# Performance work log

Measured on AMD Instinct MI355X. Metric: run time of the kernel, lower is better.

Reference implementation:

```python
import jax, jax.numpy as jnp
from jax import lax
import numpy as np

SCALE, IN_C, OUT_C, KER, R = 2, 64, 64, 3, 4

def _tconv(x, w, b, s, ker):
    # PyTorch ConvTranspose2d(w: [in,out,k,k], padding=ker//2, stride=s, output_padding=s-1)
    # as a fractionally-strided conv: flip kernel, swap in/out channel axes.
    wk = jnp.flip(jnp.transpose(w, (1, 0, 2, 3)), (2, 3))  # [out,in,k,k]
    p = ker // 2
    y = lax.conv_general_dilated(
        x, wk, window_strides=(1, 1),
        padding=[(p, p + s - 1), (p, p + s - 1)],
        lhs_dilation=(s, s),
        dimension_numbers=('NCHW', 'OIHW', 'NCHW'))
    return y + b[None, :, None, None]

def setup_inputs() -> dict:
    key = jax.random.key(0)
    ks = jax.random.split(key, 8)
    B, H, W = 4, 256, 256
    x = jax.random.normal(ks[0], (B, IN_C, H, W), jnp.float32)
    m = (jax.random.uniform(ks[1], (B, 1, H * SCALE, W * SCALE)) > 0.5).astype(jnp.float32)
    inv_mask = 1.0 - m
    # params (std per module init; exact std irrelevant for correctness)
    high_w = jax.random.normal(ks[2], (IN_C, OUT_C, KER, KER), jnp.float32) * 0.001
    high_b = jnp.zeros((OUT_C,), jnp.float32)
    low1_w = jax.random.normal(ks[3], (IN_C // R, IN_C, 1, 1), jnp.float32) * np.sqrt(2.0 / (IN_C // R))
    low1_b = jnp.zeros((IN_C // R,), jnp.float32)
    low2_w = jax.random.normal(ks[4], (IN_C // R, OUT_C, KER, KER), jnp.float32) * 0.001
    low2_b = jnp.zeros((OUT_C,), jnp.float32)
    return {"x": x, "mask": m, "inv_mask": inv_mask,
            "high_w": high_w, "high_b": high_b,
            "low1_w": low1_w, "low1_b": low1_b,
            "low2_w": low2_w, "low2_b": low2_b}

def reference(x, mask, inv_mask, high_w, high_b, low1_w, low1_b, low2_w, low2_b):
    # high branch: full transposed conv, masked per upsampled pixel
    high = _tconv(x, high_w, high_b, SCALE, KER) * mask  # [B,out,2H,2W]
    # low branch: 1x1 channel reduction then transposed conv, complementary mask
    low = jnp.einsum('bchw,oc->bohw', x, low1_w[:, :, 0, 0]) + low1_b[None, :, None, None]
    low = _tconv(low, low2_w, low2_b, SCALE, KER) * inv_mask
    return high + low
```

## Files before the change

### kernel.cpp

```cpp
#include <hip/hip_runtime.h>


typedef unsigned short u16;
typedef unsigned int   u32;
typedef __bf16 bf16x8 __attribute__((ext_vector_type(8)));
typedef u16    u16x8  __attribute__((ext_vector_type(8)));
typedef float  f32x4  __attribute__((ext_vector_type(4)));

#define DEV static __device__ __forceinline__

DEV u16   f2bf(float f){ u32 u = __builtin_bit_cast(u32, f); u += 0x7FFF + ((u >> 16) & 1); return (u16)(u >> 16); }
DEV bf16x8 asb(u16x8 v){ return __builtin_bit_cast(bf16x8, v); }
#define MF(acc, A, B) acc = __builtin_amdgcn_mfma_f32_16x16x32_bf16(asb(A), asb(B), acc, 0, 0, 0)

__global__ __launch_bounds__(256) void wprep(const float* __restrict__ hw, const float* __restrict__ lw,
                                             const float* __restrict__ l1w,
                                             u16* __restrict__ whi, u16* __restrict__ wlo,
                                             u16* __restrict__ w1f)
{
  int t = blockIdx.x * 256 + threadIdx.x;
  if (t < 36864) {
    int e = t & 7, lane = (t >> 3) & 63, tile = (t >> 9) & 3, Q = (t >> 11) & 1, tap = t >> 12;
    int q = lane >> 4, n = lane & 15;
    int c = 32 * Q + 8 * q + e, och = 16 * tile + n;
    whi[t] = f2bf(hw[(c * 64 + och) * 9 + tap]);
  } else if (t < 47104) {
    int t2 = t - 36864;
    int e = t2 & 7, lane = (t2 >> 3) & 63, tile = (t2 >> 9) & 3, f = t2 >> 11;
    int q = lane >> 4, n = lane & 15, och = 16 * tile + n;
    const int ta[10] = {4, -1, 3, 5, 1, 7, 0, 2, 6, 8};
    int tap = ta[f * 2 + (q >> 1)];
    u16 v = 0;
    if (tap >= 0) { int c = 8 * (q & 1) + e; v = f2bf(lw[(c * 64 + och) * 9 + tap]); }
    wlo[t2] = v;
  } else if (t < 48128) {
    int t3 = t - 47104;
    int e = t3 & 7, lane = (t3 >> 3) & 63, Q = t3 >> 9;
    int q = lane >> 4, n = lane & 15;
    w1f[t3] = f2bf(l1w[n * 64 + 32 * Q + 8 * q + e]);
  }
}

__global__ __launch_bounds__(256) void tconv_main(
    const float* __restrict__ x,
    const u16* __restrict__ whi, const u16* __restrict__ wlo, const u16* __restrict__ w1f,
    const float* __restrict__ mask, const float* __restrict__ hbp,
    const float* __restrict__ lbp, const float* __restrict__ l1bp,
    float* __restrict__ out)
{
  __shared__ __attribute__((aligned(16))) u16 xs [2][68][72];
  __shared__ __attribute__((aligned(16))) u16 xrs[2][68][24];

  const int tid  = threadIdx.x;
  const int lane = tid & 63, wid = tid >> 6;
  const int j0 = blockIdx.x * 64;
  const int i  = blockIdx.y;
  const int b  = blockIdx.z;
  const int q  = lane >> 4, n = lane & 15;

  for (int idx = tid; idx < 2 * 64 * 32; idx += 256) {
    int cp = idx & 31, c = (idx >> 5) & 63, row = idx >> 11;
    int gi = i + row, col = cp * 2;
    float2 v = make_float2(0.f, 0.f);
    if (gi < 256) v = *(const float2*)&x[((size_t)b << 22) + ((size_t)c << 16) + (gi << 8) + (j0 + col)];
    xs[row][col    ][c] = f2bf(v.x);
    xs[row][col + 1][c] = f2bf(v.y);
  }
  if (tid < 128) {
    int row = tid >> 6, c = tid & 63, gi = i + row, gj = j0 + 64;
    float v = 0.f;
    if (gi < 256 && gj < 256) v = x[((size_t)b << 22) + ((size_t)c << 16) + (gi << 8) + gj];
    xs[row][64][c] = f2bf(v);
  }
  if (tid < 136) {
    int row = tid / 68, col = tid % 68;
    *(uint4*)&xrs[row][col][16] = make_uint4(0, 0, 0, 0);
  }
  __syncthreads();

  {
    const u16x8* w1f8 = (const u16x8*)w1f;
    u16x8 aw0 = w1f8[lane], aw1 = w1f8[64 + lane];
    float b14[4];
    #pragma unroll
    for (int r = 0; r < 4; ++r) b14[r] = l1bp[4 * q + r];
    #pragma unroll
    for (int tt = 0; tt < 3; ++tt) {
      int tile = wid + 4 * tt;
      if (tile < 9) {
        int p = 16 * tile + n;
        int row = (p >= 72) ? 1 : 0;
        int col = p - 72 * row;
        int colr = (col < 68) ? col : 67;
        f32x4 d = {0.f, 0.f, 0.f, 0.f};
        MF(d, aw0, *(const u16x8*)&xs[row][colr][8 * q]);
        MF(d, aw1, *(const u16x8*)&xs[row][colr][32 + 8 * q]);
        if (col < 65) {
          int gi = i + row, gj = j0 + col;
          u32 pk0 = 0, pk1 = 0;
          if (gi < 256 && gj < 256) {
            pk0 = (u32)f2bf(d[0] + b14[0]) | ((u32)f2bf(d[1] + b14[1]) << 16);
            pk1 = (u32)f2bf(d[2] + b14[2]) | ((u32)f2bf(d[3] + b14[3]) << 16);
          }
          *(uint2*)&xrs[row][col][4 * q] = make_uint2(pk0, pk1);
        }
      }
    }
  }

  u16x8 bh[9][2], bl[5];
  {
    const u16x8* wh8 = (const u16x8*)whi;
    #pragma unroll
    for (int tap = 0; tap < 9; ++tap)
      #pragma unroll
      for (int Q = 0; Q < 2; ++Q)
        bh[tap][Q] = wh8[((tap * 2 + Q) * 4 + wid) * 64 + lane];
    const u16x8* wl8 = (const u16x8*)wlo;
    #pragma unroll
    for (int f = 0; f < 5; ++f) bl[f] = wl8[(f * 4 + wid) * 64 + lane];
  }
  float hb4[4], lb4[4];
  #pragma unroll
  for (int r = 0; r < 4; ++r) {
    hb4[r] = hbp[16 * wid + 4 * q + r];
    lb4[r] = lbp[16 * wid + 4 * q + r];
  }
  __syncthreads();

  #pragma unroll
  for (int jt = 0; jt < 64; jt += 16) {
    const int colb = jt + n;
    u16x8 ah[2][2][2];
    #pragma unroll
    for (int r = 0; r < 2; ++r)
      #pragma unroll
      for (int d = 0; d < 2; ++d)
        #pragma unroll
        for (int Q = 0; Q < 2; ++Q)
          ah[r][d][Q] = *(const u16x8*)&xs[r][colb + d][32 * Q + 8 * q];
    const int dq = (q < 2) ? 1 : 0;
    u16x8 lf0 = *(const u16x8*)&xrs[0 ][colb     ][(q < 2) ? 8 * (q & 1) : 16];
    u16x8 lf1 = *(const u16x8*)&xrs[0 ][colb + dq][8 * (q & 1)];
    u16x8 lf2 = *(const u16x8*)&xrs[dq][colb     ][8 * (q & 1)];
    u16x8 lf3 = *(const u16x8*)&xrs[1 ][colb + dq][8 * (q & 1)];

    auto epi2 = [&](f32x4 hi0, f32x4 lo0, f32x4 hi1, f32x4 lo1, int py) {
      int y  = 2 * i + py;
      int xc = 2 * (j0 + jt + n);
      float2 mk = *(const float2*)&mask[((b * 512 + y) << 9) + xc];
      #pragma unroll
      for (int reg = 0; reg < 4; ++reg) {
        int oc = 16 * wid + 4 * q + reg;
        float h0 = hi0[reg] + hb4[reg], l0 = lo0[reg] + lb4[reg];
        float h1 = hi1[reg] + hb4[reg], l1 = lo1[reg] + lb4[reg];
        float2 o;
        o.x = l0 + mk.x * (h0 - l0);
        o.y = l1 + mk.y * (h1 - l1);
        *(float2*)&out[((size_t)(b * 64 + oc) << 18) + ((size_t)y << 9) + xc] = o;
      }
    };

    const f32x4 z4 = {0.f, 0.f, 0.f, 0.f};
    f32x4 h0, l0, h1, l1;
    h0 = z4; l0 = z4;
    MF(h0, bh[4][0], ah[0][0][0]); MF(h0, bh[4][1], ah[0][0][1]);
    MF(l0, bl[0], lf0);
    h1 = z4; l1 = z4;
    MF(h1, bh[3][0], ah[0][1][0]); MF(h1, bh[3][1], ah[0][1][1]);
    MF(h1, bh[5][0], ah[0][0][0]); MF(h1, bh[5][1], ah[0][0][1]);
    MF(l1, bl[1], lf1);
    epi2(h0, l0, h1, l1, 0);
    h0 = z4; l0 = z4;
    MF(h0, bh[1][0], ah[1][0][0]); MF(h0, bh[1][1], ah[1][0][1]);
    MF(h0, bh[7][0], ah[0][0][0]); MF(h0, bh[7][1], ah[0][0][1]);
    MF(l0, bl[2], lf2);
    h1 = z4; l1 = z4;
    MF(h1, bh[0][0], ah[1][1][0]); MF(h1, bh[0][1], ah[1][1][1]);
    MF(h1, bh[2][0], ah[1][0][0]); MF(h1, bh[2][1], ah[1][0][1]);
    MF(h1, bh[6][0], ah[0][1][0]); MF(h1, bh[6][1], ah[0][1][1]);
    MF(h1, bh[8][0], ah[0][0][0]); MF(h1, bh[8][1], ah[0][0][1]);
    MF(l1, bl[3], lf3); MF(l1, bl[4], lf1);
    epi2(h0, l0, h1, l1, 1);
  }
}

extern "C" void kernel_launch(void* const* d_in, const int* in_sizes, int n_in,
                              void* d_out, int out_size, void* d_ws, size_t ws_size,
                              hipStream_t stream)
{
  const float* x    = (const float*)d_in[0];
  const float* mask = (const float*)d_in[1];
  const float* hw   = (const float*)d_in[3];
  const float* hb   = (const float*)d_in[4];
  const float* l1w  = (const float*)d_in[5];
  const float* l1b  = (const float*)d_in[6];
  const float* l2w  = (const float*)d_in[7];
  const float* l2b  = (const float*)d_in[8];
  float* out = (float*)d_out;
  u16* ws  = (u16*)d_ws;
  u16* whi = ws;
  u16* wlo = whi + 36864;
  u16* w1f = whi + 47104;

  wprep<<<188, 256, 0, stream>>>(hw, l2w, l1w, whi, wlo, w1f);
  tconv_main<<<dim3(4, 256, 4), 256, 0, stream>>>(x, whi, wlo, w1f, mask, hb, l2b, l1b, out);
}
```

Measured before the change: 411.2 us.

## Process two input rows per block to share halo rows and weight loads

Each block now handles two input rows (four output rows), loading three x rows into shared memory instead of two per row. This reduces redundant halo loads and the per-block cost of loading weights into registers, and halves the grid. It also widens the global loads to float4 and uses nontemporal stores for the output. In exchange, shared memory per block grows and there are fewer blocks available to hide latency.

```diff
diff --git a/kernel.cpp b/kernel.cpp
--- a/kernel.cpp
+++ b/kernel.cpp
@@ -6,6 +6,7 @@
 typedef __bf16 bf16x8 __attribute__((ext_vector_type(8)));
 typedef u16    u16x8  __attribute__((ext_vector_type(8)));
 typedef float  f32x4  __attribute__((ext_vector_type(4)));
+typedef float  f32x2  __attribute__((ext_vector_type(2)));
 
 #define DEV static __device__ __forceinline__
 
@@ -48,31 +49,33 @@
     const float* __restrict__ lbp, const float* __restrict__ l1bp,
     float* __restrict__ out)
 {
-  __shared__ __attribute__((aligned(16))) u16 xs [2][68][72];
-  __shared__ __attribute__((aligned(16))) u16 xrs[2][68][24];
+  __shared__ __attribute__((aligned(16))) u16 xs [3][68][72];
+  __shared__ __attribute__((aligned(16))) u16 xrs[3][68][24];
 
   const int tid  = threadIdx.x;
   const int lane = tid & 63, wid = tid >> 6;
   const int j0 = blockIdx.x * 64;
-  const int i  = blockIdx.y;
+  const int ib = blockIdx.y;
   const int b  = blockIdx.z;
   const int q  = lane >> 4, n = lane & 15;
 
-  for (int idx = tid; idx < 2 * 64 * 32; idx += 256) {
-    int cp = idx & 31, c = (idx >> 5) & 63, row = idx >> 11;
-    int gi = i + row, col = cp * 2;
-    float2 v = make_float2(0.f, 0.f);
-    if (gi < 256) v = *(const float2*)&x[((size_t)b << 22) + ((size_t)c << 16) + (gi << 8) + (j0 + col)];
+  for (int idx = tid; idx < 3 * 64 * 16; idx += 256) {
+    int f4 = idx & 15, c = (idx >> 4) & 63, row = idx >> 10;
+    int gi = 2 * ib + row, col = 4 * f4;
+    float4 v = make_float4(0.f, 0.f, 0.f, 0.f);
+    if (gi < 256) v = *(const float4*)&x[((size_t)b << 22) + ((size_t)c << 16) + (gi << 8) + (j0 + col)];
     xs[row][col    ][c] = f2bf(v.x);
     xs[row][col + 1][c] = f2bf(v.y);
-  }
-  if (tid < 128) {
-    int row = tid >> 6, c = tid & 63, gi = i + row, gj = j0 + 64;
+    xs[row][col + 2][c] = f2bf(v.z);
+    xs[row][col + 3][c] = f2bf(v.w);
+  }
+  if (tid < 192) {
+    int row = tid >> 6, c = tid & 63, gi = 2 * ib + row, gj = j0 + 64;
     float v = 0.f;
     if (gi < 256 && gj < 256) v = x[((size_t)b << 22) + ((size_t)c << 16) + (gi << 8) + gj];
     xs[row][64][c] = f2bf(v);
   }
-  if (tid < 136) {
+  if (tid < 204) {
     int row = tid / 68, col = tid % 68;
     *(uint4*)&xrs[row][col][16] = make_uint4(0, 0, 0, 0);
   }
@@ -85,18 +88,18 @@
     #pragma unroll
     for (int r = 0; r < 4; ++r) b14[r] = l1bp[4 * q + r];
     #pragma unroll
-    for (int tt = 0; tt < 3; ++tt) {
+    for (int tt = 0; tt < 4; ++tt) {
       int tile = wid + 4 * tt;
-      if (tile < 9) {
+      if (tile < 14) {
         int p = 16 * tile + n;
-        int row = (p >= 72) ? 1 : 0;
+        int row = (p >= 144) ? 2 : ((p >= 72) ? 1 : 0);
         int col = p - 72 * row;
         int colr = (col < 68) ? col : 67;
         f32x4 d = {0.f, 0.f, 0.f, 0.f};
         MF(d, aw0, *(const u16x8*)&xs[row][colr][8 * q]);
         MF(d, aw1, *(const u16x8*)&xs[row][colr][32 + 8 * q]);
         if (col < 65) {
-          int gi = i + row, gj = j0 + col;
+          int gi = 2 * ib + row, gj = j0 + col;
           u32 pk0 = 0, pk1 = 0;
           if (gi < 256 && gj < 256) {
             pk0 = (u32)f2bf(d[0] + b14[0]) | ((u32)f2bf(d[1] + b14[1]) << 16);
@@ -128,60 +131,63 @@
   }
   __syncthreads();
 
-  #pragma unroll
-  for (int jt = 0; jt < 64; jt += 16) {
-    const int colb = jt + n;
-    u16x8 ah[2][2][2];
-    #pragma unroll
-    for (int r = 0; r < 2; ++r)
+  #pragma unroll 1
+  for (int iv = 0; iv < 2; ++iv) {
+    #pragma unroll
+    for (int jt = 0; jt < 64; jt += 16) {
+      const int colb = jt + n;
+      u16x8 ah[2][2][2];
       #pragma unroll
-      for (int d = 0; d < 2; ++d)
+      for (int r = 0; r < 2; ++r)
         #pragma unroll
-        for (int Q = 0; Q < 2; ++Q)
-          ah[r][d][Q] = *(const u16x8*)&xs[r][colb + d][32 * Q + 8 * q];
-    const int dq = (q < 2) ? 1 : 0;
-    u16x8 lf0 = *(const u16x8*)&xrs[0 ][colb     ][(q < 2) ? 8 * (q & 1) : 16];
-    u16x8 lf1 = *(const u16x8*)&xrs[0 ][colb + dq][8 * (q & 1)];
-    u16x8 lf2 = *(const u16x8*)&xrs[dq][colb     ][8 * (q & 1)];
-    u16x8 lf3 = *(const u16x8*)&xrs[1 ][colb + dq][8 * (q & 1)];
-
-    auto epi2 = [&](f32x4 hi0, f32x4 lo0, f32x4 hi1, f32x4 lo1, int py) {
-      int y  = 2 * i + py;
-      int xc = 2 * (j0 + jt + n);
-      float2 mk = *(const float2*)&mask[((b * 512 + y) << 9) + xc];
-      #pragma unroll
-      for (int reg = 0; reg < 4; ++reg) {
-        int oc = 16 * wid + 4 * q + reg;
-        float h0 = hi0[reg] + hb4[reg], l0 = lo0[reg] + lb4[reg];
-        float h1 = hi1[reg] + hb4[reg], l1 = lo1[reg] + lb4[reg];
-        float2 o;
-        o.x = l0 + mk.x * (h0 - l0);
-        o.y = l1 + mk.y * (h1 - l1);
-        *(float2*)&out[((size_t)(b * 64 + oc) << 18) + ((size_t)y << 9) + xc] = o;
-      }
-    };
-
-    const f32x4 z4 = {0.f, 0.f, 0.f, 0.f};
-    f32x4 h0, l0, h1, l1;
-    h0 = z4; l0 = z4;
-    MF(h0, bh[4][0], ah[0][0][0]); MF(h0, bh[4][1], ah[0][0][1]);
-    MF(l0, bl[0], lf0);
-    h1 = z4; l1 = z4;
-    MF(h1, bh[3][0], ah[0][1][0]); MF(h1, bh[3][1], ah[0][1][1]);
-    MF(h1, bh[5][0], ah[0][0][0]); MF(h1, bh[5][1], ah[0][0][1]);
-    MF(l1, bl[1], lf1);
-    epi2(h0, l0, h1, l1, 0);
-    h0 = z4; l0 = z4;
-    MF(h0, bh[1][0], ah[1][0][0]); MF(h0, bh[1][1], ah[1][0][1]);
-    MF(h0, bh[7][0], ah[0][0][0]); MF(h0, bh[7][1], ah[0][0][1]);
-    MF(l0, bl[2], lf2);
-    h1 = z4; l1 = z4;
-    MF(h1, bh[0][0], ah[1][1][0]); MF(h1, bh[0][1], ah[1][1][1]);
-    MF(h1, bh[2][0], ah[1][0][0]); MF(h1, bh[2][1], ah[1][0][1]);
-    MF(h1, bh[6][0], ah[0][1][0]); MF(h1, bh[6][1], ah[0][1][1]);
-    MF(h1, bh[8][0], ah[0][0][0]); MF(h1, bh[8][1], ah[0][0][1]);
-    MF(l1, bl[3], lf3); MF(l1, bl[4], lf1);
-    epi2(h0, l0, h1, l1, 1);
+        for (int d = 0; d < 2; ++d)
+          #pragma unroll
+          for (int Q = 0; Q < 2; ++Q)
+            ah[r][d][Q] = *(const u16x8*)&xs[iv + r][colb + d][32 * Q + 8 * q];
+      const int dq = (q < 2) ? 1 : 0;
+      u16x8 lf0 = *(const u16x8*)&xrs[iv     ][colb     ][(q < 2) ? 8 * (q & 1) : 16];
+      u16x8 lf1 = *(const u16x8*)&xrs[iv     ][colb + dq][8 * (q & 1)];
+      u16x8 lf2 = *(const u16x8*)&xrs[iv + dq][colb     ][8 * (q & 1)];
+      u16x8 lf3 = *(const u16x8*)&xrs[iv + 1 ][colb + dq][8 * (q & 1)];
+
+      auto epi2 = [&](f32x4 hi0, f32x4 lo0, f32x4 hi1, f32x4 lo1, int py) {
+        int y  = 4 * ib + 2 * iv + py;
+        int xc = 2 * (j0 + jt + n);
+        float2 mk = *(const float2*)&mask[((b * 512 + y) << 9) + xc];
+        #pragma unroll
+        for (int reg = 0; reg < 4; ++reg) {
+          int oc = 16 * wid + 4 * q + reg;
+          float h0 = hi0[reg] + hb4[reg], l0 = lo0[reg] + lb4[reg];
+          float h1 = hi1[reg] + hb4[reg], l1 = lo1[reg] + lb4[reg];
+          f32x2 o;
+          o.x = l0 + mk.x * (h0 - l0);
+          o.y = l1 + mk.y * (h1 - l1);
+          __builtin_nontemporal_store(o, (f32x2*)&out[((size_t)(b * 64 + oc) << 18) + ((size_t)y << 9) + xc]);
+        }
+      };
+
+      const f32x4 z4 = {0.f, 0.f, 0.f, 0.f};
+      f32x4 h0, l0, h1, l1;
+      h0 = z4; l0 = z4;
+      MF(h0, bh[4][0], ah[0][0][0]); MF(h0, bh[4][1], ah[0][0][1]);
+      MF(l0, bl[0], lf0);
+      h1 = z4; l1 = z4;
+      MF(h1, bh[3][0], ah[0][1][0]); MF(h1, bh[3][1], ah[0][1][1]);
+      MF(h1, bh[5][0], ah[0][0][0]); MF(h1, bh[5][1], ah[0][0][1]);
+      MF(l1, bl[1], lf1);
+      epi2(h0, l0, h1, l1, 0);
+      h0 = z4; l0 = z4;
+      MF(h0, bh[1][0], ah[1][0][0]); MF(h0, bh[1][1], ah[1][0][1]);
+      MF(h0, bh[7][0], ah[0][0][0]); MF(h0, bh[7][1], ah[0][0][1]);
+      MF(l0, bl[2], lf2);
+      h1 = z4; l1 = z4;
+      MF(h1, bh[0][0], ah[1][1][0]); MF(h1, bh[0][1], ah[1][1][1]);
+      MF(h1, bh[2][0], ah[1][0][0]); MF(h1, bh[2][1], ah[1][0][1]);
+      MF(h1, bh[6][0], ah[0][1][0]); MF(h1, bh[6][1], ah[0][1][1]);
+      MF(h1, bh[8][0], ah[0][0][0]); MF(h1, bh[8][1], ah[0][0][1]);
+      MF(l1, bl[3], lf3); MF(l1, bl[4], lf1);
+      epi2(h0, l0, h1, l1, 1);
+    }
   }
 }
 
@@ -204,5 +210,5 @@
   u16* w1f = whi + 47104;
 
   wprep<<<188, 256, 0, stream>>>(hw, l2w, l1w, whi, wlo, w1f);
-  tconv_main<<<dim3(4, 256, 4), 256, 0, stream>>>(x, whi, wlo, w1f, mask, hb, l2b, l1b, out);
+  tconv_main<<<dim3(4, 128, 4), 256, 0, stream>>>(x, whi, wlo, w1f, mask, hb, l2b, l1b, out);
 }
```

New measurement: 372.8 us. 1.1x faster.
